# Optimization experiments

Hardware: AMD Instinct MI355X
Metric: run time of the kernel (lower is better)

Reference implementation:

```python
import jax, jax.numpy as jnp
import numpy as np

B, P, V, E, F = 4, 8, 2048, 2048, 4096
BIG = 1e10  # stand-in for +inf that keeps gradients clean


def setup_inputs() -> dict:
    key = jax.random.key(0)
    ks = jax.random.split(key, 8)
    xs = jax.random.normal(ks[0], (B, V, 3), jnp.float32)
    # Projection matrices: random rows for x/y, third (depth) row kept near
    # [0,0,0,2] so the perspective divide is well conditioned for randn verts.
    pm = 0.5 * jax.random.normal(ks[1], (P, 3, 4), jnp.float32)
    pm = pm.at[:, 2, :3].set(0.01 * jax.random.normal(ks[2], (P, 3), jnp.float32))
    pm = pm.at[:, 2, 3].set(2.0)
    edgemaps = jax.random.normal(ks[3], (B, P, E, 2), jnp.float32)
    edgemap_lengths = jax.random.randint(ks[4], (B, P), E // 2, E + 1)
    boundary_mask = jax.random.randint(ks[5], (B, P, V), 0, 2).astype(bool)
    faces = jax.random.randint(ks[6], (B, F, 3), 0, V)
    target_volumes = 10.0 * jax.random.normal(ks[7], (B,), jnp.float32)
    return dict(xs=xs, projmatrices=pm, edgemaps=edgemaps,
                edgemap_lengths=edgemap_lengths, boundary_mask=boundary_mask,
                faces=faces, target_volumes=target_volumes)


def _silhouette_chamfer(xs, projmatrices, edgemaps, edgemap_lengths, boundary_mask):
    b, v, _ = xs.shape
    xh = jnp.concatenate([xs, jnp.ones((b, v, 1), xs.dtype)], axis=-1)  # [B,V,4]
    proj = jnp.einsum('pij,bvj->bpvi', projmatrices, xh)               # [B,P,V,3]
    pts = proj[..., :2] / proj[..., 2:3]                               # [B,P,V,2]
    e = edgemaps.shape[2]
    d2 = (jnp.sum(pts * pts, -1)[..., :, None]
          + jnp.sum(edgemaps * edgemaps, -1)[..., None, :]
          - 2.0 * jnp.einsum('bpvc,bpec->bpve', pts, edgemaps))
    yvalid = jnp.arange(e)[None, None, :] < edgemap_lengths[..., None]  # [B,P,E]
    d2 = jnp.where(yvalid[:, :, None, :], d2, jnp.asarray(BIG, d2.dtype))
    mins = jnp.min(d2, axis=-1)                                        # [B,P,V]
    xm = boundary_mask.astype(d2.dtype)
    # point_reduction='mean' over valid boundary points per projection,
    # batch_reduction='mean' over the P projections of each mesh.
    per_proj = jnp.sum(mins * xm, -1) / jnp.maximum(jnp.sum(xm, -1), 1.0)  # [B,P]
    return jnp.mean(per_proj, axis=-1)                                 # [B]


def _volume_constraint(xs, faces, target_volumes):
    b = xs.shape[0]
    fv = xs[jnp.arange(b)[:, None, None], faces]   # [B,F,3,3] gather face verts
    v0, v1, v2 = fv[:, :, 0], fv[:, :, 1], fv[:, :, 2]
    face_vols = jnp.sum(jnp.cross(v0, v1) * v2, axis=-1) / 6.0  # [B,F]
    vols = jnp.abs(jnp.sum(face_vols, axis=-1))                 # scatter-add per mesh
    return (vols - target_volumes) ** 2                          # [B]


def reference(xs, projmatrices, edgemaps, edgemap_lengths, boundary_mask, faces, target_volumes):
    chamfer = _silhouette_chamfer(xs, projmatrices, edgemaps, edgemap_lengths, boundary_mask)
    vol_error = _volume_constraint(xs, faces, target_volumes)
    return chamfer, vol_error
```

## Files before the change

kernel.cpp:

```cpp
#include <hip/hip_runtime.h>

#define NB 4
#define NP 8
#define NV 2048
#define NE 2048
#define NF 4096
#define BIGV 1.0e10f
#define NCOMBO (NB * NP)
#define NSPAN 16
#define SPANE 128
#define SPAD (SPANE + 1)
#define NVC 16
#define VC 128
#define PPAD (VC + 4)


__global__ __launch_bounds__(256) void fused_k1(
    const float* __restrict__ xs, const float* __restrict__ pm,
    const float* __restrict__ edgemaps, const int* __restrict__ elen,
    const int* __restrict__ faces, const void* __restrict__ maskp,
    float* __restrict__ spart, float* __restrict__ cpart,
    float* __restrict__ volpart)
{
    __shared__ float4 eds[NSPAN * SPAD];
    __shared__ float part[NSPAN][PPAD];
    __shared__ float reds[2], redc[2], redv[4];
    const int tid = threadIdx.x;
    const int bid = blockIdx.x;

    if (bid < 512) {
        const int combo  = bid >> 4;
        const int vchunk = bid & 15;
        const int b = combo >> 3;
        const int p = combo & 7;

        const int len = elen[combo];
        #pragma unroll
        for (int j = 0; j < 8; j++) {
            const int e = tid + (j << 8);
            float2 exy = ((const float2*)edgemaps)[(size_t)combo * NE + e];
            float e2;
            if (e < len) {
                e2 = exy.x * exy.x + exy.y * exy.y;
            } else {
                exy.x = 0.0f; exy.y = 0.0f; e2 = BIGV;
            }
            eds[(e >> 7) * SPAD + (e & 127)] = make_float4(exy.x, exy.y, e2, 0.0f);
        }

        const float* M = pm + p * 12;
        const float m00 = M[0], m01 = M[1], m02 = M[2],  m03 = M[3];
        const float m10 = M[4], m11 = M[5], m12 = M[6],  m13 = M[7];
        const float m20 = M[8], m21 = M[9], m22 = M[10], m23 = M[11];

        const int vgroup = tid & 15;
        const int span   = tid >> 4;
        const int v0     = vchunk * VC + (vgroup << 3);

        float px2[8], py2[8], v2[8], mn[8];
        #pragma unroll
        for (int i = 0; i < 8; i++) {
            const int v = v0 + i;
            const float x = xs[((size_t)b * NV + v) * 3 + 0];
            const float y = xs[((size_t)b * NV + v) * 3 + 1];
            const float z = xs[((size_t)b * NV + v) * 3 + 2];
            const float r0 = m00 * x + m01 * y + m02 * z + m03;
            const float r1 = m10 * x + m11 * y + m12 * z + m13;
            const float r2 = m20 * x + m21 * y + m22 * z + m23;
            const float inv = 1.0f / r2;
            const float px = r0 * inv;
            const float py = r1 * inv;
            px2[i] = -2.0f * px;
            py2[i] = -2.0f * py;
            v2[i]  = px * px + py * py;
            mn[i]  = 3.0e38f;
        }
        __syncthreads();

        const float4* ep = eds + span * SPAD;
        #pragma unroll 4
        for (int k = 0; k < SPANE; k++) {
            const float4 ed = ep[k];
            #pragma unroll
            for (int i = 0; i < 8; i++)
                mn[i] = fminf(mn[i], fmaf(py2[i], ed.y, fmaf(px2[i], ed.x, ed.z)));
        }

        #pragma unroll
        for (int i = 0; i < 8; i++)
            part[span][(vgroup << 3) + i] = mn[i] + v2[i];

        const unsigned* mw = (const unsigned*)maskp;
        bool as_int = true;
        #pragma unroll
        for (int k = 0; k < 16; k++)
            if (mw[k] > 1u) as_int = false;

        __syncthreads();

        float s = 0.0f, c = 0.0f;
        if (tid < VC) {
            float m = part[0][tid];
            #pragma unroll
            for (int sp = 1; sp < NSPAN; sp++)
                m = fminf(m, part[sp][tid]);
            const size_t mix = (size_t)combo * NV + vchunk * VC + tid;
            const float msk = as_int ? (((const int*)maskp)[mix] ? 1.0f : 0.0f)
                                     : (((const unsigned char*)maskp)[mix] ? 1.0f : 0.0f);
            s = m * msk;
            c = msk;
        }
        #pragma unroll
        for (int off = 32; off > 0; off >>= 1) {
            s += __shfl_down(s, off);
            c += __shfl_down(c, off);
        }
        if (tid < VC && (tid & 63) == 0) { reds[tid >> 6] = s; redc[tid >> 6] = c; }
        __syncthreads();
        if (tid == 0) {
            spart[bid] = reds[0] + reds[1];
            cpart[bid] = redc[0] + redc[1];
        }
    } else {
        const int j = bid - 512;
        const int b = j >> 4;
        const int f = ((j & 15) << 8) + tid;
        const int* fc = faces + ((size_t)b * NF + f) * 3;
        const int i0 = fc[0], i1 = fc[1], i2 = fc[2];
        const float* xb = xs + (size_t)b * NV * 3;
        const float ax = xb[i0 * 3 + 0], ay = xb[i0 * 3 + 1], az = xb[i0 * 3 + 2];
        const float bx = xb[i1 * 3 + 0], by = xb[i1 * 3 + 1], bz = xb[i1 * 3 + 2];
        const float cx = xb[i2 * 3 + 0], cy = xb[i2 * 3 + 1], cz = xb[i2 * 3 + 2];
        const float crx = ay * bz - az * by;
        const float cry = az * bx - ax * bz;
        const float crz = ax * by - ay * bx;
        float fv = (crx * cx + cry * cy + crz * cz) * (1.0f / 6.0f);

        #pragma unroll
        for (int off = 32; off > 0; off >>= 1) fv += __shfl_down(fv, off);
        const int lane = tid & 63, w = tid >> 6;
        if (lane == 0) redv[w] = fv;
        __syncthreads();
        if (tid == 0) volpart[j] = redv[0] + redv[1] + redv[2] + redv[3];
    }
}

__global__ __launch_bounds__(64) void fused_k2(
    const float* __restrict__ spart, const float* __restrict__ cpart,
    const float* __restrict__ volpart, const float* __restrict__ tv,
    float* __restrict__ out)
{
    __shared__ float pc[NCOMBO];
    const int tid = threadIdx.x;
    if (tid < NCOMBO) {
        float S = 0.0f, C = 0.0f;
        #pragma unroll
        for (int k = 0; k < NVC; k++) {
            S += spart[tid * NVC + k];
            C += cpart[tid * NVC + k];
        }
        pc[tid] = S / fmaxf(C, 1.0f);
    }
    __syncthreads();
    if (tid < NB) {
        float a = 0.0f;
        #pragma unroll
        for (int p = 0; p < NP; p++) a += pc[tid * NP + p];
        out[tid] = a * (1.0f / NP);
        float vs = 0.0f;
        #pragma unroll
        for (int k = 0; k < 16; k++) vs += volpart[tid * 16 + k];
        const float d = fabsf(vs) - tv[tid];
        out[4 + tid] = d * d;
    }
}

extern "C" void kernel_launch(void* const* d_in, const int* in_sizes, int n_in,
                              void* d_out, int out_size, void* d_ws, size_t ws_size,
                              hipStream_t stream)
{
    const float* xs       = (const float*)d_in[0];
    const float* pm       = (const float*)d_in[1];
    const float* edgemaps = (const float*)d_in[2];
    const int*   elen     = (const int*)d_in[3];
    const void*  mask     = d_in[4];
    const int*   faces    = (const int*)d_in[5];
    const float* tv       = (const float*)d_in[6];
    float* out = (float*)d_out;

    float* spart   = (float*)d_ws;
    float* cpart   = spart + NCOMBO * NVC;
    float* volpart = cpart + NCOMBO * NVC;

    fused_k1<<<dim3(576), dim3(256), 0, stream>>>(xs, pm, edgemaps, elen, faces, mask,
                                                  spart, cpart, volpart);
    fused_k2<<<dim3(1), dim3(64), 0, stream>>>(spart, cpart, volpart, tv, out);
}
```

Before: 81.41 us.

## Fuse finalize via cooperative grid sync and fold volume work into chamfer blocks

Replaces the two-kernel launch with a single cooperative kernel that computes per-block partial sums, syncs the grid, and has block 0 do the final reduction, falling back to two launches if the cooperative launch fails. The separate volume blocks are removed; each of the 512 chamfer blocks now also handles 32 faces. Edge data loads become float4-vectorised with split xy/e2 shared arrays, and the inner loop processes four edges per iteration. Vertex loads use float4. The grid sync adds barrier cost and requires all 512 blocks to be co-resident.

```diff
diff --git a/kernel.cpp b/kernel.cpp
--- a/kernel.cpp
+++ b/kernel.cpp
@@ -1,4 +1,7 @@
 #include <hip/hip_runtime.h>
+#include <hip/hip_cooperative_groups.h>
+
+namespace cg = cooperative_groups;
 
 #define NB 4
 #define NP 8
@@ -8,171 +11,205 @@
 #define BIGV 1.0e10f
 #define NCOMBO (NB * NP)
 #define NSPAN 16
-#define SPANE 128
-#define SPAD (SPANE + 1)
 #define NVC 16
 #define VC 128
-#define PPAD (VC + 4)
-
-
-__global__ __launch_bounds__(256) void fused_k1(
+#define NBLK (NCOMBO * NVC)
+#define XPAD 65
+#define EPAD 132
+#define PPAD 132
+
+
+__device__ __forceinline__ void finalize_out(
+    const float* __restrict__ spart, const float* __restrict__ cpart,
+    const float* __restrict__ volpart, const float* __restrict__ tv,
+    float* __restrict__ out, const int tid)
+{
+    __shared__ float pc[NCOMBO];
+    __shared__ float rv[4];
+    if (tid < NCOMBO) {
+        const float4* s4 = (const float4*)(spart + (tid << 4));
+        const float4* c4 = (const float4*)(cpart + (tid << 4));
+        float S = 0.0f, C = 0.0f;
+        #pragma unroll
+        for (int j = 0; j < 4; j++) {
+            const float4 a = s4[j], d = c4[j];
+            S += (a.x + a.y) + (a.z + a.w);
+            C += (d.x + d.y) + (d.z + d.w);
+        }
+        pc[tid] = S / fmaxf(C, 1.0f);
+    }
+    const int w = tid >> 6, lane = tid & 63;
+    float vs = volpart[(w << 7) + lane] + volpart[(w << 7) + 64 + lane];
+    #pragma unroll
+    for (int off = 32; off > 0; off >>= 1) vs += __shfl_down(vs, off);
+    if (lane == 0) rv[w] = vs;
+    __syncthreads();
+    if (tid < NB) {
+        float a = 0.0f;
+        #pragma unroll
+        for (int q = 0; q < NP; q++) a += pc[tid * NP + q];
+        out[tid] = a * (1.0f / NP);
+        const float d = fabsf(rv[tid]) - tv[tid];
+        out[4 + tid] = d * d;
+    }
+}
+
+template <int COOP>
+__global__ __launch_bounds__(256) void fused_all(
     const float* __restrict__ xs, const float* __restrict__ pm,
     const float* __restrict__ edgemaps, const int* __restrict__ elen,
     const int* __restrict__ faces, const void* __restrict__ maskp,
+    const float* __restrict__ tv,
     float* __restrict__ spart, float* __restrict__ cpart,
-    float* __restrict__ volpart)
-{
-    __shared__ float4 eds[NSPAN * SPAD];
-    __shared__ float part[NSPAN][PPAD];
-    __shared__ float reds[2], redc[2], redv[4];
+    float* __restrict__ volpart, float* __restrict__ out)
+{
+    __shared__ __align__(16) float4 eds_xy[NSPAN * XPAD];
+    __shared__ __align__(16) float  e2a[NSPAN * EPAD];
+    __shared__ __align__(16) float  part[NSPAN * PPAD];
+    __shared__ float reds[2], redc[2];
     const int tid = threadIdx.x;
     const int bid = blockIdx.x;
-
-    if (bid < 512) {
-        const int combo  = bid >> 4;
-        const int vchunk = bid & 15;
-        const int b = combo >> 3;
-        const int p = combo & 7;
-
-        const int len = elen[combo];
-        #pragma unroll
-        for (int j = 0; j < 8; j++) {
-            const int e = tid + (j << 8);
-            float2 exy = ((const float2*)edgemaps)[(size_t)combo * NE + e];
-            float e2;
-            if (e < len) {
-                e2 = exy.x * exy.x + exy.y * exy.y;
-            } else {
-                exy.x = 0.0f; exy.y = 0.0f; e2 = BIGV;
-            }
-            eds[(e >> 7) * SPAD + (e & 127)] = make_float4(exy.x, exy.y, e2, 0.0f);
-        }
-
-        const float* M = pm + p * 12;
-        const float m00 = M[0], m01 = M[1], m02 = M[2],  m03 = M[3];
-        const float m10 = M[4], m11 = M[5], m12 = M[6],  m13 = M[7];
-        const float m20 = M[8], m21 = M[9], m22 = M[10], m23 = M[11];
-
-        const int vgroup = tid & 15;
-        const int span   = tid >> 4;
-        const int v0     = vchunk * VC + (vgroup << 3);
-
-        float px2[8], py2[8], v2[8], mn[8];
-        #pragma unroll
-        for (int i = 0; i < 8; i++) {
-            const int v = v0 + i;
-            const float x = xs[((size_t)b * NV + v) * 3 + 0];
-            const float y = xs[((size_t)b * NV + v) * 3 + 1];
-            const float z = xs[((size_t)b * NV + v) * 3 + 2];
-            const float r0 = m00 * x + m01 * y + m02 * z + m03;
-            const float r1 = m10 * x + m11 * y + m12 * z + m13;
-            const float r2 = m20 * x + m21 * y + m22 * z + m23;
-            const float inv = 1.0f / r2;
-            const float px = r0 * inv;
-            const float py = r1 * inv;
-            px2[i] = -2.0f * px;
-            py2[i] = -2.0f * py;
-            v2[i]  = px * px + py * py;
-            mn[i]  = 3.0e38f;
-        }
-        __syncthreads();
-
-        const float4* ep = eds + span * SPAD;
-        #pragma unroll 4
-        for (int k = 0; k < SPANE; k++) {
-            const float4 ed = ep[k];
-            #pragma unroll
-            for (int i = 0; i < 8; i++)
-                mn[i] = fminf(mn[i], fmaf(py2[i], ed.y, fmaf(px2[i], ed.x, ed.z)));
-        }
-
-        #pragma unroll
-        for (int i = 0; i < 8; i++)
-            part[span][(vgroup << 3) + i] = mn[i] + v2[i];
-
-        const unsigned* mw = (const unsigned*)maskp;
-        bool as_int = true;
-        #pragma unroll
-        for (int k = 0; k < 16; k++)
-            if (mw[k] > 1u) as_int = false;
-
-        __syncthreads();
-
-        float s = 0.0f, c = 0.0f;
-        if (tid < VC) {
-            float m = part[0][tid];
-            #pragma unroll
-            for (int sp = 1; sp < NSPAN; sp++)
-                m = fminf(m, part[sp][tid]);
-            const size_t mix = (size_t)combo * NV + vchunk * VC + tid;
-            const float msk = as_int ? (((const int*)maskp)[mix] ? 1.0f : 0.0f)
-                                     : (((const unsigned char*)maskp)[mix] ? 1.0f : 0.0f);
-            s = m * msk;
-            c = msk;
-        }
-        #pragma unroll
-        for (int off = 32; off > 0; off >>= 1) {
-            s += __shfl_down(s, off);
-            c += __shfl_down(c, off);
-        }
-        if (tid < VC && (tid & 63) == 0) { reds[tid >> 6] = s; redc[tid >> 6] = c; }
-        __syncthreads();
-        if (tid == 0) {
-            spart[bid] = reds[0] + reds[1];
-            cpart[bid] = redc[0] + redc[1];
-        }
-    } else {
-        const int j = bid - 512;
-        const int b = j >> 4;
-        const int f = ((j & 15) << 8) + tid;
-        const int* fc = faces + ((size_t)b * NF + f) * 3;
+    const int combo  = bid >> 4;
+    const int vchunk = bid & 15;
+    const int b = combo >> 3;
+    const int p = combo & 7;
+
+    const int len = elen[combo];
+    const float4* emapf4 = (const float4*)(edgemaps + (size_t)combo * NE * 2);
+    #pragma unroll
+    for (int j = 0; j < 4; j++) {
+        const int t = tid + (j << 8);
+        float4 f4 = emapf4[t];
+        const int e0 = t << 1;
+        float a2, b2;
+        if (e0 < len)     { a2 = f4.x * f4.x + f4.y * f4.y; }
+        else              { f4.x = 0.0f; f4.y = 0.0f; a2 = BIGV; }
+        if (e0 + 1 < len) { b2 = f4.z * f4.z + f4.w * f4.w; }
+        else              { f4.z = 0.0f; f4.w = 0.0f; b2 = BIGV; }
+        const int sp = t >> 6, pr = t & 63;
+        eds_xy[sp * XPAD + pr] = f4;
+        e2a[sp * EPAD + (pr << 1) + 0] = a2;
+        e2a[sp * EPAD + (pr << 1) + 1] = b2;
+    }
+
+    const float* M = pm + p * 12;
+    const float m00 = M[0], m01 = M[1], m02 = M[2],  m03 = M[3];
+    const float m10 = M[4], m11 = M[5], m12 = M[6],  m13 = M[7];
+    const float m20 = M[8], m21 = M[9], m22 = M[10], m23 = M[11];
+
+    const int vgroup = tid & 15;
+    const int span   = tid >> 4;
+    const int v0     = vchunk * VC + (vgroup << 3);
+
+    float c24[24];
+    {
+        const float4* xv = (const float4*)(xs + ((size_t)b * NV + v0) * 3);
+        #pragma unroll
+        for (int j = 0; j < 6; j++) ((float4*)c24)[j] = xv[j];
+    }
+    float px2[8], py2[8], v2[8], mn[8];
+    #pragma unroll
+    for (int i = 0; i < 8; i++) {
+        const float x = c24[3 * i], y = c24[3 * i + 1], z = c24[3 * i + 2];
+        const float r0 = m00 * x + m01 * y + m02 * z + m03;
+        const float r1 = m10 * x + m11 * y + m12 * z + m13;
+        const float r2 = m20 * x + m21 * y + m22 * z + m23;
+        const float inv = 1.0f / r2;
+        const float px = r0 * inv;
+        const float py = r1 * inv;
+        px2[i] = -2.0f * px;
+        py2[i] = -2.0f * py;
+        v2[i]  = px * px + py * py;
+        mn[i]  = 3.0e38f;
+    }
+
+    float fvol = 0.0f;
+    if (tid < 32) {
+        const int f = (bid << 5) + tid;
+        const int* fc = faces + (size_t)f * 3;
         const int i0 = fc[0], i1 = fc[1], i2 = fc[2];
-        const float* xb = xs + (size_t)b * NV * 3;
-        const float ax = xb[i0 * 3 + 0], ay = xb[i0 * 3 + 1], az = xb[i0 * 3 + 2];
-        const float bx = xb[i1 * 3 + 0], by = xb[i1 * 3 + 1], bz = xb[i1 * 3 + 2];
-        const float cx = xb[i2 * 3 + 0], cy = xb[i2 * 3 + 1], cz = xb[i2 * 3 + 2];
+        const float* xb = xs + (size_t)(f >> 12) * NV * 3;
+        const float ax = xb[i0 * 3], ay = xb[i0 * 3 + 1], az = xb[i0 * 3 + 2];
+        const float bx = xb[i1 * 3], by = xb[i1 * 3 + 1], bz = xb[i1 * 3 + 2];
+        const float cx = xb[i2 * 3], cy = xb[i2 * 3 + 1], cz = xb[i2 * 3 + 2];
         const float crx = ay * bz - az * by;
         const float cry = az * bx - ax * bz;
         const float crz = ax * by - ay * bx;
-        float fv = (crx * cx + cry * cy + crz * cz) * (1.0f / 6.0f);
-
-        #pragma unroll
-        for (int off = 32; off > 0; off >>= 1) fv += __shfl_down(fv, off);
-        const int lane = tid & 63, w = tid >> 6;
-        if (lane == 0) redv[w] = fv;
-        __syncthreads();
-        if (tid == 0) volpart[j] = redv[0] + redv[1] + redv[2] + redv[3];
-    }
-}
-
-__global__ __launch_bounds__(64) void fused_k2(
+        fvol = (crx * cx + cry * cy + crz * cz) * (1.0f / 6.0f);
+    }
+    __syncthreads();
+
+    const float4* xp = eds_xy + span * XPAD;
+    const float*  ep = e2a + span * EPAD;
+    #pragma unroll 2
+    for (int k = 0; k < 32; k++) {
+        const float4 xy01 = xp[2 * k];
+        const float4 xy23 = xp[2 * k + 1];
+        const float4 ee   = *(const float4*)(ep + 4 * k);
+        #pragma unroll
+        for (int i = 0; i < 8; i++) {
+            const float d0 = fmaf(py2[i], xy01.y, fmaf(px2[i], xy01.x, ee.x));
+            const float d1 = fmaf(py2[i], xy01.w, fmaf(px2[i], xy01.z, ee.y));
+            const float d2 = fmaf(py2[i], xy23.y, fmaf(px2[i], xy23.x, ee.z));
+            const float d3 = fmaf(py2[i], xy23.w, fmaf(px2[i], xy23.z, ee.w));
+            mn[i] = fminf(fminf(mn[i], d0), d1);
+            mn[i] = fminf(fminf(mn[i], d2), d3);
+        }
+    }
+
+    #pragma unroll
+    for (int i = 0; i < 8; i++)
+        part[span * PPAD + (vgroup << 3) + i] = mn[i] + v2[i];
+
+    const unsigned* mw = (const unsigned*)maskp;
+    bool as_int = true;
+    #pragma unroll
+    for (int k = 0; k < 16; k++)
+        if (mw[k] > 1u) as_int = false;
+
+    __syncthreads();
+    float s = 0.0f, c = 0.0f;
+    if (tid < VC) {
+        float m = part[tid];
+        #pragma unroll
+        for (int sp = 1; sp < NSPAN; sp++)
+            m = fminf(m, part[sp * PPAD + tid]);
+        const size_t mix = (size_t)combo * NV + vchunk * VC + tid;
+        const float msk = as_int ? (((const int*)maskp)[mix] ? 1.0f : 0.0f)
+                                 : (((const unsigned char*)maskp)[mix] ? 1.0f : 0.0f);
+        s = m * msk;
+        c = msk;
+    }
+    #pragma unroll
+    for (int off = 32; off > 0; off >>= 1) {
+        s += __shfl_down(s, off);
+        c += __shfl_down(c, off);
+    }
+    if (tid < VC && (tid & 63) == 0) { reds[tid >> 6] = s; redc[tid >> 6] = c; }
+
+    #pragma unroll
+    for (int off = 32; off > 0; off >>= 1) fvol += __shfl_down(fvol, off);
+
+    __syncthreads();
+    if (tid == 0) {
+        spart[bid]   = reds[0] + reds[1];
+        cpart[bid]   = redc[0] + redc[1];
+        volpart[bid] = fvol;
+    }
+
+    if (COOP) {
+        __threadfence();
+        cg::this_grid().sync();
+        if (bid == 0) finalize_out(spart, cpart, volpart, tv, out, tid);
+    }
+}
+
+__global__ __launch_bounds__(256) void finalize_k(
     const float* __restrict__ spart, const float* __restrict__ cpart,
     const float* __restrict__ volpart, const float* __restrict__ tv,
     float* __restrict__ out)
 {
-    __shared__ float pc[NCOMBO];
-    const int tid = threadIdx.x;
-    if (tid < NCOMBO) {
-        float S = 0.0f, C = 0.0f;
-        #pragma unroll
-        for (int k = 0; k < NVC; k++) {
-            S += spart[tid * NVC + k];
-            C += cpart[tid * NVC + k];
-        }
-        pc[tid] = S / fmaxf(C, 1.0f);
-    }
-    __syncthreads();
-    if (tid < NB) {
-        float a = 0.0f;
-        #pragma unroll
-        for (int p = 0; p < NP; p++) a += pc[tid * NP + p];
-        out[tid] = a * (1.0f / NP);
-        float vs = 0.0f;
-        #pragma unroll
-        for (int k = 0; k < 16; k++) vs += volpart[tid * 16 + k];
-        const float d = fabsf(vs) - tv[tid];
-        out[4 + tid] = d * d;
-    }
+    finalize_out(spart, cpart, volpart, tv, out, threadIdx.x);
 }
 
 extern "C" void kernel_launch(void* const* d_in, const int* in_sizes, int n_in,
@@ -189,10 +226,17 @@
     float* out = (float*)d_out;
 
     float* spart   = (float*)d_ws;
-    float* cpart   = spart + NCOMBO * NVC;
-    float* volpart = cpart + NCOMBO * NVC;
-
-    fused_k1<<<dim3(576), dim3(256), 0, stream>>>(xs, pm, edgemaps, elen, faces, mask,
-                                                  spart, cpart, volpart);
-    fused_k2<<<dim3(1), dim3(64), 0, stream>>>(spart, cpart, volpart, tv, out);
-}
+    float* cpart   = spart + NBLK;
+    float* volpart = cpart + NBLK;
+
+    void* args[] = { (void*)&xs, (void*)&pm, (void*)&edgemaps, (void*)&elen,
+                     (void*)&faces, (void*)&mask, (void*)&tv,
+                     (void*)&spart, (void*)&cpart, (void*)&volpart, (void*)&out };
+    hipError_t err = hipLaunchCooperativeKernel(fused_all<1>, dim3(NBLK), dim3(256),
+                                                args, 0, stream);
+    if (err != hipSuccess) {
+        fused_all<0><<<dim3(NBLK), dim3(256), 0, stream>>>(
+            xs, pm, edgemaps, elen, faces, mask, tv, spart, cpart, volpart, out);
+        finalize_k<<<dim3(1), dim3(256), 0, stream>>>(spart, cpart, volpart, tv, out);
+    }
+}
```

Result: slower. 161.4 us (+98.2%).
